# Optimization experiments

Measured on AMD Instinct MI355X. Metric: run time of the kernel, lower is better.

The kernel has to match this reference:

```python
import jax, jax.numpy as jnp
import numpy as np

NB = 16   # num_blocks
DIN = 64  # per-block input dim
DOUT = 64 # per-block output dim
NT = 2    # n_templates (ns)


def setup_inputs() -> dict:
    key = jax.random.key(0)
    k1, k2, k3, k4, k5 = jax.random.split(key, 5)
    T, B = 2048, 8
    a = 0.1  # GroupLinearLayer init range
    x = jax.random.normal(k1, (T, B, NB * DIN), dtype=jnp.float32)
    module_emb = 0.1 * jax.random.normal(k2, (1, 1, NB * DIN), dtype=jnp.float32)
    read_w = jax.random.uniform(k3, (1, DIN, NT), dtype=jnp.float32, minval=-a, maxval=a)
    lim = 1.0 / np.sqrt(DIN)  # nn.Linear default init range
    w_stack = jax.random.uniform(k4, (NT, DOUT, DIN), dtype=jnp.float32, minval=-lim, maxval=lim)
    b_stack = jax.random.uniform(k5, (NT, DOUT), dtype=jnp.float32, minval=-lim, maxval=lim)
    return {"x": x, "module_emb": module_emb, "read_w": read_w,
            "w_stack": w_stack, "b_stack": b_stack}


def reference(x, module_emb, read_w, w_stack, b_stack):
    T, B, D = x.shape
    # add module embedding (broadcast over T, B)
    new_x = x + module_emb
    # flatten to per-block tokens: (N, DIN) with N = T*B*NB
    xf = new_x.reshape(T * B * NB, DIN)
    # routing logits via GroupLinearLayer with 1 block: (N, NT)
    logits = xf @ read_w[0]
    att = jax.nn.softmax(logits, axis=-1)
    # apply each template Linear: (N, NT, DOUT)
    x_next = jnp.einsum('nd,tod->nto', xf, w_stack) + b_stack[None, :, :]
    # soft combine templates; mean over singleton dim is identity
    out = jnp.einsum('nt,nto->no', att, x_next)
    return out.reshape(T, B, NB * DOUT)
```

## Files before the change

kernel.cpp:

```cpp
#include <hip/hip_runtime.h>


#define NTOK   262144
#define GPW    4
#define NBLK   1024

typedef short bf16x8 __attribute__((ext_vector_type(8)));
typedef float f32x4  __attribute__((ext_vector_type(4)));

__device__ __forceinline__ short f2bf(float f) {
    unsigned u = __float_as_uint(f);
    u += 0x7fffu + ((u >> 16) & 1u);
    return (short)(u >> 16);
}

__global__ __launch_bounds__(256) void sgll_kernel(
    const float* __restrict__ x,
    const float* __restrict__ emb,
    const float* __restrict__ rw,
    const float* __restrict__ ws,
    const float* __restrict__ bs,
    float* __restrict__ out)
{
    __shared__ float2 rp[64];
    const int tid = threadIdx.x;
    if (tid < 64) rp[tid] = make_float2(rw[2 * tid], rw[2 * tid + 1]);

    const int lane = tid & 63;
    const int wv   = tid >> 6;
    const int col  = lane & 15;
    const int q    = lane >> 4;

    bf16x8 B1[2][4], Bd[2][4];
    #pragma unroll
    for (int kt = 0; kt < 2; ++kt) {
        #pragma unroll
        for (int nt = 0; nt < 4; ++nt) {
            const int o = nt * 16 + col;
            const float* p0 = ws + o * 64 + kt * 32 + q * 8;
            const float* p1 = p0 + 4096;
            float4 a0 = *(const float4*)p0;
            float4 a1 = *(const float4*)(p0 + 4);
            float4 c0 = *(const float4*)p1;
            float4 c1 = *(const float4*)(p1 + 4);
            bf16x8 f1, fd;
            f1[0] = f2bf(c0.x); f1[1] = f2bf(c0.y); f1[2] = f2bf(c0.z); f1[3] = f2bf(c0.w);
            f1[4] = f2bf(c1.x); f1[5] = f2bf(c1.y); f1[6] = f2bf(c1.z); f1[7] = f2bf(c1.w);
            fd[0] = f2bf(a0.x - c0.x); fd[1] = f2bf(a0.y - c0.y);
            fd[2] = f2bf(a0.z - c0.z); fd[3] = f2bf(a0.w - c0.w);
            fd[4] = f2bf(a1.x - c1.x); fd[5] = f2bf(a1.y - c1.y);
            fd[6] = f2bf(a1.z - c1.z); fd[7] = f2bf(a1.w - c1.w);
            B1[kt][nt] = f1;
            Bd[kt][nt] = fd;
        }
    }

    float4 e0, e1, e2, e3;
    {
        const float* ep = emb + col * 64 + q * 8;
        e0 = *(const float4*)ep;        e1 = *(const float4*)(ep + 4);
        e2 = *(const float4*)(ep + 32); e3 = *(const float4*)(ep + 36);
    }

    float b1v[4], dbv[4];
    #pragma unroll
    for (int nt = 0; nt < 4; ++nt) {
        const int o = nt * 16 + col;
        float t1 = bs[64 + o];
        b1v[nt] = t1;
        dbv[nt] = bs[o] - t1;
    }

    __syncthreads();

    const int gw = blockIdx.x * 4 + wv;
    const size_t tok0 = (size_t)gw * (GPW * 16);

    float4 cx0, cx1, cx2, cx3;
    {
        const float* xp = x + (tok0 + col) * 64 + q * 8;
        cx0 = *(const float4*)xp;        cx1 = *(const float4*)(xp + 4);
        cx2 = *(const float4*)(xp + 32); cx3 = *(const float4*)(xp + 36);
    }

    #pragma unroll
    for (int i = 0; i < GPW; ++i) {
        float4 nx0, nx1, nx2, nx3;
        if (i + 1 < GPW) {
            const float* xp = x + (tok0 + (size_t)(i + 1) * 16 + col) * 64 + q * 8;
            nx0 = *(const float4*)xp;        nx1 = *(const float4*)(xp + 4);
            nx2 = *(const float4*)(xp + 32); nx3 = *(const float4*)(xp + 36);
        }

        float xv[16];
        xv[0]  = cx0.x + e0.x; xv[1]  = cx0.y + e0.y; xv[2]  = cx0.z + e0.z; xv[3]  = cx0.w + e0.w;
        xv[4]  = cx1.x + e1.x; xv[5]  = cx1.y + e1.y; xv[6]  = cx1.z + e1.z; xv[7]  = cx1.w + e1.w;
        xv[8]  = cx2.x + e2.x; xv[9]  = cx2.y + e2.y; xv[10] = cx2.z + e2.z; xv[11] = cx2.w + e2.w;
        xv[12] = cx3.x + e3.x; xv[13] = cx3.y + e3.y; xv[14] = cx3.z + e3.z; xv[15] = cx3.w + e3.w;

        float l0 = 0.f, l1 = 0.f;
        #pragma unroll
        for (int j = 0; j < 8; ++j) {
            float2 r = rp[q * 8 + j];
            l0 = fmaf(xv[j], r.x, l0);
            l1 = fmaf(xv[j], r.y, l1);
        }
        #pragma unroll
        for (int j = 0; j < 8; ++j) {
            float2 r = rp[32 + q * 8 + j];
            l0 = fmaf(xv[8 + j], r.x, l0);
            l1 = fmaf(xv[8 + j], r.y, l1);
        }
        l0 += __shfl_xor(l0, 16); l0 += __shfl_xor(l0, 32);
        l1 += __shfl_xor(l1, 16); l1 += __shfl_xor(l1, 32);
        const float att = 1.0f / (1.0f + __expf(l1 - l0));

        bf16x8 A0, A1;
        #pragma unroll
        for (int j = 0; j < 8; ++j) {
            A0[j] = f2bf(xv[j]);
            A1[j] = f2bf(xv[8 + j]);
        }

        f32x4 aY[4], aD[4];
        #pragma unroll
        for (int nt = 0; nt < 4; ++nt) {
            f32x4 z = {0.f, 0.f, 0.f, 0.f};
            f32x4 y = __builtin_amdgcn_mfma_f32_16x16x32_bf16(A0, B1[0][nt], z, 0, 0, 0);
            y       = __builtin_amdgcn_mfma_f32_16x16x32_bf16(A1, B1[1][nt], y, 0, 0, 0);
            f32x4 d = __builtin_amdgcn_mfma_f32_16x16x32_bf16(A0, Bd[0][nt], z, 0, 0, 0);
            d       = __builtin_amdgcn_mfma_f32_16x16x32_bf16(A1, Bd[1][nt], d, 0, 0, 0);
            aY[nt] = y;
            aD[nt] = d;
        }

        const size_t rowtok = tok0 + (size_t)i * 16;
        #pragma unroll
        for (int r = 0; r < 4; ++r) {
            const int row = q * 4 + r;
            const float attr = __shfl(att, row);
            float* op = out + (rowtok + row) * 64 + col;
            #pragma unroll
            for (int nt = 0; nt < 4; ++nt) {
                op[nt * 16] = aY[nt][r] + b1v[nt] + attr * (aD[nt][r] + dbv[nt]);
            }
        }

        if (i + 1 < GPW) { cx0 = nx0; cx1 = nx1; cx2 = nx2; cx3 = nx3; }
    }
}

extern "C" void kernel_launch(void* const* d_in, const int* in_sizes, int n_in,
                              void* d_out, int out_size, void* d_ws, size_t ws_size,
                              hipStream_t stream) {
    const float* x   = (const float*)d_in[0];
    const float* emb = (const float*)d_in[1];
    const float* rw  = (const float*)d_in[2];
    const float* wsk = (const float*)d_in[3];
    const float* bs  = (const float*)d_in[4];
    float* out = (float*)d_out;

    sgll_kernel<<<NBLK, 256, 0, stream>>>(x, emb, rw, wsk, bs, out);
}
```

Before: 139.0 us.

## Fold embedding and bias into MFMA accumulator init, routing logits via MFMA

The per-token embedding add and the bias terms are replaced by precomputed accumulator initial values: W·emb+b is computed once per block with MFMA and stored in shared memory. The routing logits are also computed with MFMA instead of FMAs and shuffles. Weights move from registers to shared memory, the GEMM is transposed so each lane writes float4 rows, and a cheaper round-half-up bf16 pack via perm replaces round-to-nearest-even. It also adds triple-buffered x loads and an occupancy hint in launch bounds. The goal is to cut VALU work and scalar stores, at the cost of extra LDS reads, an extra barrier, and a slightly different rounding mode.

Result: faster. 132.0 us (-5.0%).

```diff
diff --git a/kernel.cpp b/kernel.cpp
--- a/kernel.cpp
+++ b/kernel.cpp
@@ -1,20 +1,25 @@
 #include <hip/hip_runtime.h>
 
 
-#define NTOK   262144
-#define GPW    4
-#define NBLK   1024
+#define NBLK 1024
 
 typedef short bf16x8 __attribute__((ext_vector_type(8)));
 typedef float f32x4  __attribute__((ext_vector_type(4)));
 
-__device__ __forceinline__ short f2bf(float f) {
-    unsigned u = __float_as_uint(f);
-    u += 0x7fffu + ((u >> 16) & 1u);
-    return (short)(u >> 16);
+union B8 { bf16x8 v; unsigned u[4]; };
+
+__device__ __forceinline__ unsigned pk2bf(float lo, float hi) {
+    unsigned a = __float_as_uint(lo) + 0x8000u;
+    unsigned b = __float_as_uint(hi) + 0x8000u;
+    return __builtin_amdgcn_perm(b, a, 0x07060302u);
 }
 
-__global__ __launch_bounds__(256) void sgll_kernel(
+__device__ __forceinline__ void pack8(B8& d, float4 p, float4 q) {
+    d.u[0] = pk2bf(p.x, p.y); d.u[1] = pk2bf(p.z, p.w);
+    d.u[2] = pk2bf(q.x, q.y); d.u[3] = pk2bf(q.z, q.w);
+}
+
+__global__ __launch_bounds__(256, 4) void sgll_kernel(
     const float* __restrict__ x,
     const float* __restrict__ emb,
     const float* __restrict__ rw,
@@ -22,132 +27,122 @@
     const float* __restrict__ bs,
     float* __restrict__ out)
 {
-    __shared__ float2 rp[64];
-    const int tid = threadIdx.x;
-    if (tid < 64) rp[tid] = make_float2(rw[2 * tid], rw[2 * tid + 1]);
+    __shared__ bf16x8 sW1[8][64];
+    __shared__ bf16x8 sWd[8][64];
+    __shared__ f32x4  sI1[4][64];
+    __shared__ f32x4  sId[4][64];
+    __shared__ f32x4  sIl[64];
 
+    const int tid  = threadIdx.x;
     const int lane = tid & 63;
     const int wv   = tid >> 6;
     const int col  = lane & 15;
     const int q    = lane >> 4;
 
-    bf16x8 B1[2][4], Bd[2][4];
     #pragma unroll
-    for (int kt = 0; kt < 2; ++kt) {
-        #pragma unroll
-        for (int nt = 0; nt < 4; ++nt) {
-            const int o = nt * 16 + col;
-            const float* p0 = ws + o * 64 + kt * 32 + q * 8;
-            const float* p1 = p0 + 4096;
-            float4 a0 = *(const float4*)p0;
-            float4 a1 = *(const float4*)(p0 + 4);
-            float4 c0 = *(const float4*)p1;
-            float4 c1 = *(const float4*)(p1 + 4);
-            bf16x8 f1, fd;
-            f1[0] = f2bf(c0.x); f1[1] = f2bf(c0.y); f1[2] = f2bf(c0.z); f1[3] = f2bf(c0.w);
-            f1[4] = f2bf(c1.x); f1[5] = f2bf(c1.y); f1[6] = f2bf(c1.z); f1[7] = f2bf(c1.w);
-            fd[0] = f2bf(a0.x - c0.x); fd[1] = f2bf(a0.y - c0.y);
-            fd[2] = f2bf(a0.z - c0.z); fd[3] = f2bf(a0.w - c0.w);
-            fd[4] = f2bf(a1.x - c1.x); fd[5] = f2bf(a1.y - c1.y);
-            fd[6] = f2bf(a1.z - c1.z); fd[7] = f2bf(a1.w - c1.w);
-            B1[kt][nt] = f1;
-            Bd[kt][nt] = fd;
-        }
+    for (int c = wv; c < 8; c += 4) {
+        const int kt = c >> 2, ot = c & 3;
+        const float* p0 = ws + (ot * 16 + col) * 64 + kt * 32 + q * 8;
+        const float* p1 = p0 + 4096;
+        float4 a0 = *(const float4*)p0, a1 = *(const float4*)(p0 + 4);
+        float4 c0 = *(const float4*)p1, c1 = *(const float4*)(p1 + 4);
+        B8 f1, fd;
+        pack8(f1, make_float4(c0.x, c0.y, c0.z, c0.w), c1);
+        fd.u[0] = pk2bf(a0.x - c0.x, a0.y - c0.y);
+        fd.u[1] = pk2bf(a0.z - c0.z, a0.w - c0.w);
+        fd.u[2] = pk2bf(a1.x - c1.x, a1.y - c1.y);
+        fd.u[3] = pk2bf(a1.z - c1.z, a1.w - c1.w);
+        sW1[c][lane] = f1.v;
+        sWd[c][lane] = fd.v;
     }
 
-    float4 e0, e1, e2, e3;
+    B8 R0, R1;
     {
-        const float* ep = emb + col * 64 + q * 8;
-        e0 = *(const float4*)ep;        e1 = *(const float4*)(ep + 4);
-        e2 = *(const float4*)(ep + 32); e3 = *(const float4*)(ep + 36);
-    }
-
-    float b1v[4], dbv[4];
-    #pragma unroll
-    for (int nt = 0; nt < 4; ++nt) {
-        const int o = nt * 16 + col;
-        float t1 = bs[64 + o];
-        b1v[nt] = t1;
-        dbv[nt] = bs[o] - t1;
+        float v[8];
+        #pragma unroll
+        for (int j = 0; j < 8; ++j)
+            v[j] = (col < 2) ? rw[(q * 8 + j) * 2 + col] : 0.f;
+        pack8(R0, make_float4(v[0], v[1], v[2], v[3]), make_float4(v[4], v[5], v[6], v[7]));
+        #pragma unroll
+        for (int j = 0; j < 8; ++j)
+            v[j] = (col < 2) ? rw[(32 + q * 8 + j) * 2 + col] : 0.f;
+        pack8(R1, make_float4(v[0], v[1], v[2], v[3]), make_float4(v[4], v[5], v[6], v[7]));
     }
 
     __syncthreads();
 
-    const int gw = blockIdx.x * 4 + wv;
-    const size_t tok0 = (size_t)gw * (GPW * 16);
+    if (wv == 0) {
+        const float* ep = emb + col * 64 + q * 8;
+        float4 e0 = *(const float4*)ep,        e1 = *(const float4*)(ep + 4);
+        float4 e2 = *(const float4*)(ep + 32), e3 = *(const float4*)(ep + 36);
+        B8 E0, E1;
+        pack8(E0, e0, e1);
+        pack8(E1, e2, e3);
+        #pragma unroll
+        for (int ot = 0; ot < 4; ++ot) {
+            float4 b1 = *(const float4*)(bs + 64 + ot * 16 + q * 4);
+            float4 b0 = *(const float4*)(bs + ot * 16 + q * 4);
+            f32x4 a1 = {b1.x, b1.y, b1.z, b1.w};
+            f32x4 ad = {b0.x - b1.x, b0.y - b1.y, b0.z - b1.z, b0.w - b1.w};
+            a1 = __builtin_amdgcn_mfma_f32_16x16x32_bf16(sW1[ot][lane],     E0.v, a1, 0, 0, 0);
+            a1 = __builtin_amdgcn_mfma_f32_16x16x32_bf16(sW1[4 + ot][lane], E1.v, a1, 0, 0, 0);
+            ad = __builtin_amdgcn_mfma_f32_16x16x32_bf16(sWd[ot][lane],     E0.v, ad, 0, 0, 0);
+            ad = __builtin_amdgcn_mfma_f32_16x16x32_bf16(sWd[4 + ot][lane], E1.v, ad, 0, 0, 0);
+            sI1[ot][lane] = a1;
+            sId[ot][lane] = ad;
+        }
+        f32x4 zl = {0.f, 0.f, 0.f, 0.f};
+        zl = __builtin_amdgcn_mfma_f32_16x16x32_bf16(R0.v, E0.v, zl, 0, 0, 0);
+        zl = __builtin_amdgcn_mfma_f32_16x16x32_bf16(R1.v, E1.v, zl, 0, 0, 0);
+        sIl[lane] = zl;
+    }
+    __syncthreads();
 
-    float4 cx0, cx1, cx2, cx3;
-    {
-        const float* xp = x + (tok0 + col) * 64 + q * 8;
-        cx0 = *(const float4*)xp;        cx1 = *(const float4*)(xp + 4);
-        cx2 = *(const float4*)(xp + 32); cx3 = *(const float4*)(xp + 36);
-    }
+    const long base = (long)(blockIdx.x * 4 + wv) * 64;
+    float4 A[3][4];
+
+    #define LOAD_TILE(buf, t)  do {                                        \
+        const float* p = x + (base + (long)(t) * 16 + col) * 64 + q * 8;   \
+        A[buf][0] = *(const float4*)p;        A[buf][1] = *(const float4*)(p + 4);  \
+        A[buf][2] = *(const float4*)(p + 32); A[buf][3] = *(const float4*)(p + 36); \
+    } while (0)
+
+    LOAD_TILE(0, 0);
+    LOAD_TILE(1, 1);
 
     #pragma unroll
-    for (int i = 0; i < GPW; ++i) {
-        float4 nx0, nx1, nx2, nx3;
-        if (i + 1 < GPW) {
-            const float* xp = x + (tok0 + (size_t)(i + 1) * 16 + col) * 64 + q * 8;
-            nx0 = *(const float4*)xp;        nx1 = *(const float4*)(xp + 4);
-            nx2 = *(const float4*)(xp + 32); nx3 = *(const float4*)(xp + 36);
+    for (int i = 0; i < 4; ++i) {
+        const int b = i % 3;
+        if (i + 2 < 4) LOAD_TILE((i + 2) % 3, i + 2);
+
+        B8 X0, X1;
+        pack8(X0, A[b][0], A[b][1]);
+        pack8(X1, A[b][2], A[b][3]);
+
+        f32x4 lac = sIl[lane];
+        lac = __builtin_amdgcn_mfma_f32_16x16x32_bf16(R0.v, X0.v, lac, 0, 0, 0);
+        lac = __builtin_amdgcn_mfma_f32_16x16x32_bf16(R1.v, X1.v, lac, 0, 0, 0);
+        float att = 1.0f / (1.0f + __expf(lac[1] - lac[0]));
+        att = __shfl(att, col);
+
+        const long rowoff = (base + (long)i * 16 + col) * 64;
+        #pragma unroll
+        for (int ot = 0; ot < 4; ++ot) {
+            f32x4 y = sI1[ot][lane];
+            y = __builtin_amdgcn_mfma_f32_16x16x32_bf16(sW1[ot][lane],     X0.v, y, 0, 0, 0);
+            y = __builtin_amdgcn_mfma_f32_16x16x32_bf16(sW1[4 + ot][lane], X1.v, y, 0, 0, 0);
+            f32x4 d = sId[ot][lane];
+            d = __builtin_amdgcn_mfma_f32_16x16x32_bf16(sWd[ot][lane],     X0.v, d, 0, 0, 0);
+            d = __builtin_amdgcn_mfma_f32_16x16x32_bf16(sWd[4 + ot][lane], X1.v, d, 0, 0, 0);
+            float4 o;
+            o.x = fmaf(att, d[0], y[0]);
+            o.y = fmaf(att, d[1], y[1]);
+            o.z = fmaf(att, d[2], y[2]);
+            o.w = fmaf(att, d[3], y[3]);
+            *(float4*)(out + rowoff + ot * 16 + q * 4) = o;
         }
-
-        float xv[16];
-        xv[0]  = cx0.x + e0.x; xv[1]  = cx0.y + e0.y; xv[2]  = cx0.z + e0.z; xv[3]  = cx0.w + e0.w;
-        xv[4]  = cx1.x + e1.x; xv[5]  = cx1.y + e1.y; xv[6]  = cx1.z + e1.z; xv[7]  = cx1.w + e1.w;
-        xv[8]  = cx2.x + e2.x; xv[9]  = cx2.y + e2.y; xv[10] = cx2.z + e2.z; xv[11] = cx2.w + e2.w;
-        xv[12] = cx3.x + e3.x; xv[13] = cx3.y + e3.y; xv[14] = cx3.z + e3.z; xv[15] = cx3.w + e3.w;
-
-        float l0 = 0.f, l1 = 0.f;
-        #pragma unroll
-        for (int j = 0; j < 8; ++j) {
-            float2 r = rp[q * 8 + j];
-            l0 = fmaf(xv[j], r.x, l0);
-            l1 = fmaf(xv[j], r.y, l1);
-        }
-        #pragma unroll
-        for (int j = 0; j < 8; ++j) {
-            float2 r = rp[32 + q * 8 + j];
-            l0 = fmaf(xv[8 + j], r.x, l0);
-            l1 = fmaf(xv[8 + j], r.y, l1);
-        }
-        l0 += __shfl_xor(l0, 16); l0 += __shfl_xor(l0, 32);
-        l1 += __shfl_xor(l1, 16); l1 += __shfl_xor(l1, 32);
-        const float att = 1.0f / (1.0f + __expf(l1 - l0));
-
-        bf16x8 A0, A1;
-        #pragma unroll
-        for (int j = 0; j < 8; ++j) {
-            A0[j] = f2bf(xv[j]);
-            A1[j] = f2bf(xv[8 + j]);
-        }
-
-        f32x4 aY[4], aD[4];
-        #pragma unroll
-        for (int nt = 0; nt < 4; ++nt) {
-            f32x4 z = {0.f, 0.f, 0.f, 0.f};
-            f32x4 y = __builtin_amdgcn_mfma_f32_16x16x32_bf16(A0, B1[0][nt], z, 0, 0, 0);
-            y       = __builtin_amdgcn_mfma_f32_16x16x32_bf16(A1, B1[1][nt], y, 0, 0, 0);
-            f32x4 d = __builtin_amdgcn_mfma_f32_16x16x32_bf16(A0, Bd[0][nt], z, 0, 0, 0);
-            d       = __builtin_amdgcn_mfma_f32_16x16x32_bf16(A1, Bd[1][nt], d, 0, 0, 0);
-            aY[nt] = y;
-            aD[nt] = d;
-        }
-
-        const size_t rowtok = tok0 + (size_t)i * 16;
-        #pragma unroll
-        for (int r = 0; r < 4; ++r) {
-            const int row = q * 4 + r;
-            const float attr = __shfl(att, row);
-            float* op = out + (rowtok + row) * 64 + col;
-            #pragma unroll
-            for (int nt = 0; nt < 4; ++nt) {
-                op[nt * 16] = aY[nt][r] + b1v[nt] + attr * (aD[nt][r] + dbv[nt]);
-            }
-        }
-
-        if (i + 1 < GPW) { cx0 = nx0; cx1 = nx1; cx2 = nx2; cx3 = nx3; }
     }
+    #undef LOAD_TILE
 }
 
 extern "C" void kernel_launch(void* const* d_in, const int* in_sizes, int n_in,
@@ -159,6 +154,5 @@
     const float* wsk = (const float*)d_in[3];
     const float* bs  = (const float*)d_in[4];
     float* out = (float*)d_out;
-
     sgll_kernel<<<NBLK, 256, 0, stream>>>(x, emb, rw, wsk, bs, out);
 }
```
